# Kernel optimization log

Measured on AMD Instinct MI355X. Metric: run time of the kernel, lower is better.

Reference implementation:

```python
import jax, jax.numpy as jnp
import numpy as np

N = 100000   # nodes per type
E = 400000   # edges per relation
D = 128      # in_dim == out_dim
H = 4        # heads
DK = D // H  # 32
EPS = 1e-5


def setup_inputs() -> dict:
    key = jax.random.key(0)
    ks = jax.random.split(key, 16)
    s = 1.0 / np.sqrt(D)  # fan-in scaling for stable activations
    inp = {
        "x_drug": jax.random.normal(ks[0], (N, D), jnp.float32),
        "x_dis": jax.random.normal(ks[1], (N, D), jnp.float32),
        "Wp_drug": jax.random.normal(ks[2], (D, D), jnp.float32) * s,
        "bp_drug": jnp.zeros((D,), jnp.float32),
        "Wp_dis": jax.random.normal(ks[3], (D, D), jnp.float32) * s,
        "bp_dis": jnp.zeros((D,), jnp.float32),
        "Wk_r0": jax.random.normal(ks[4], (D, D), jnp.float32) * s,
        "Wv_r0": jax.random.normal(ks[5], (D, D), jnp.float32) * s,
        "Wk_r1": jax.random.normal(ks[6], (D, D), jnp.float32) * s,
        "Wv_r1": jax.random.normal(ks[7], (D, D), jnp.float32) * s,
        "Wu_drug": jax.random.normal(ks[8], (D, D), jnp.float32) * s,
        "bu_drug": jnp.zeros((D,), jnp.float32),
        "Wu_dis": jax.random.normal(ks[9], (D, D), jnp.float32) * s,
        "bu_dis": jnp.zeros((D,), jnp.float32),
        "g_drug": jnp.ones((D,), jnp.float32),
        "be_drug": jnp.zeros((D,), jnp.float32),
        "g_dis": jnp.ones((D,), jnp.float32),
        "be_dis": jnp.zeros((D,), jnp.float32),
        "ei_r0": jax.random.randint(ks[10], (2, E), 0, N, jnp.int32),  # drug -> dis
        "ei_r1": jax.random.randint(ks[11], (2, E), 0, N, jnp.int32),  # dis  -> drug
    }
    return inp


def _rel_attention(h_src_all, h_dst_all, ei, Wk, Wv, n_dst):
    # gather -> per-relation K/V proj -> edge softmax over dst -> scatter-add
    src, dst = ei[0], ei[1]
    h_src = h_src_all[src]                                  # [E, D]
    Q = h_dst_all[dst].reshape(-1, H, DK)                   # [E, H, DK]
    K = (h_src @ Wk).reshape(-1, H, DK)
    V = (h_src @ Wv).reshape(-1, H, DK)
    scores = jnp.sum(Q * K, axis=-1) / np.sqrt(DK)          # [E, H]
    # scatter_softmax over destination groups (numerically stable)
    m = jax.lax.stop_gradient(
        jax.ops.segment_max(scores, dst, num_segments=n_dst))  # [N, H]
    ex = jnp.exp(scores - m[dst])
    ssum = jax.ops.segment_sum(ex, dst, num_segments=n_dst)    # [N, H]
    attn = ex / ssum[dst]                                      # [E, H]
    wV = (V * attn[..., None]).reshape(-1, D)                  # [E, D]
    return jax.ops.segment_sum(wV, dst, num_segments=n_dst)    # [N, D]


def _update(h, agg, Wu, bu, g, be):
    x = h + (agg @ Wu + bu)  # skip + update (dropout=0)
    mu = jnp.mean(x, axis=-1, keepdims=True)
    var = jnp.var(x, axis=-1, keepdims=True)
    ln = (x - mu) * jax.lax.rsqrt(var + EPS) * g + be
    return jax.nn.relu(ln)


def reference(x_drug, x_dis, Wp_drug, bp_drug, Wp_dis, bp_dis,
              Wk_r0, Wv_r0, Wk_r1, Wv_r1,
              Wu_drug, bu_drug, Wu_dis, bu_dis,
              g_drug, be_drug, g_dis, be_dis, ei_r0, ei_r1):
    # type-specific projection
    h_drug = x_drug @ Wp_drug + bp_drug
    h_dis = x_dis @ Wp_dis + bp_dis
    # per-relation attention + intra/inter-type aggregation
    agg_dis = _rel_attention(h_drug, h_dis, ei_r0, Wk_r0, Wv_r0, N)
    agg_drug = _rel_attention(h_dis, h_drug, ei_r1, Wk_r1, Wv_r1, N)
    out_drug = _update(h_drug, agg_drug, Wu_drug, bu_drug, g_drug, be_drug)
    out_dis = _update(h_dis, agg_dis, Wu_dis, bu_dis, g_dis, be_dis)
    return jnp.stack([out_drug, out_dis])  # [2, N, D]
```

## Files before the change

### kernel.cpp

```cpp
#include <hip/hip_runtime.h>
#include <math.h>

#define NN 100000
#define EE 400000
#define DD 128

typedef __attribute__((ext_vector_type(8))) short bf16x8;
typedef __attribute__((ext_vector_type(4))) float f32x4;

#if defined(__has_builtin)
#if __has_builtin(__builtin_amdgcn_fdot2_f32_bf16)
#define HAVE_FDOT2 1
typedef __attribute__((ext_vector_type(2))) __bf16 bf16x2t;
#endif
#endif

__device__ __forceinline__ unsigned short f2bf(float f) {
  unsigned u = __float_as_uint(f);
  u += 0x7FFF + ((u >> 16) & 1);
  return (unsigned short)(u >> 16);
}
__device__ __forceinline__ float bf2f(unsigned short u) {
  return __uint_as_float(((unsigned)u) << 16);
}

__global__ __launch_bounds__(256) void prep_weights(
    const float* __restrict__ Wp_dr, const float* __restrict__ bp_dr,
    const float* __restrict__ Wp_di, const float* __restrict__ bp_di,
    const float* __restrict__ Wu_dr, const float* __restrict__ Wu_di,
    const float* __restrict__ Bk0, const float* __restrict__ Bv0,
    const float* __restrict__ Bk1, const float* __restrict__ Bv1,
    unsigned short* __restrict__ Wpt_dr, unsigned short* __restrict__ Wpt_di,
    unsigned short* __restrict__ Wut_dr, unsigned short* __restrict__ Wut_di,
    unsigned short* __restrict__ Wkt0, float* __restrict__ bk0,
    unsigned short* __restrict__ Wvt0, float* __restrict__ bv0,
    unsigned short* __restrict__ Wkt1, float* __restrict__ bk1,
    unsigned short* __restrict__ Wvt1, float* __restrict__ bv1) {
  const int b = blockIdx.x, t = threadIdx.x;
  if (b < 256) {
    const int id = b * 256 + t;
    const int m = id >> 14, rem = id & 16383, k = rem & 127, c = rem >> 7;
    const float* W = (m == 0) ? Wp_dr : (m == 1) ? Wp_di : (m == 2) ? Wu_dr : Wu_di;
    unsigned short* O = (m == 0) ? Wpt_dr : (m == 1) ? Wpt_di : (m == 2) ? Wut_dr : Wut_di;
    O[c * DD + k] = f2bf(W[(size_t)k * DD + c]);
  } else if (b < 512) {
    const int id = (b - 256) * 256 + t;
    const int m = id >> 14, rem = id & 16383, k = rem & 127, c = rem >> 7;
    const float* A = (m < 2) ? Wp_dr : Wp_di;
    const float* B = (m == 0) ? Bk0 : (m == 1) ? Bv0 : (m == 2) ? Bk1 : Bv1;
    unsigned short* O = (m == 0) ? Wkt0 : (m == 1) ? Wvt0 : (m == 2) ? Wkt1 : Wvt1;
    const float4* a4 = (const float4*)(A + (size_t)k * DD);
    float s = 0.0f;
#pragma unroll 8
    for (int j4 = 0; j4 < 32; ++j4) {
      const float4 av = a4[j4];
      s += av.x * B[(4 * j4 + 0) * DD + c] + av.y * B[(4 * j4 + 1) * DD + c]
         + av.z * B[(4 * j4 + 2) * DD + c] + av.w * B[(4 * j4 + 3) * DD + c];
    }
    O[c * DD + k] = f2bf(s);
  } else {
    const int id = (b - 512) * 256 + t;
    if (id < 512) {
      const int m = id >> 7, c = id & 127;
      const float* bp = (m < 2) ? bp_dr : bp_di;
      const float* B = (m == 0) ? Bk0 : (m == 1) ? Bv0 : (m == 2) ? Bk1 : Bv1;
      float* bo = (m == 0) ? bk0 : (m == 1) ? bv0 : (m == 2) ? bk1 : bv1;
      float s = 0.0f;
#pragma unroll 8
      for (int j = 0; j < DD; ++j) s += bp[j] * B[j * DD + c];
      bo[c] = s;
    }
  }
}

#define STAGE_W(SRC)                                                          \
  do {                                                                        \
    __syncthreads();                                                          \
    _Pragma("unroll") for (int i_ = threadIdx.x; i_ < 2048; i_ += 256) {      \
      const int L_ = i_ * 16;                                                 \
      *(float4*)((char*)WL + (L_ ^ (((L_ >> 8) & 7) << 4))) =                 \
          ((const float4*)(SRC))[i_];                                         \
    }                                                                         \
    __syncthreads();                                                          \
  } while (0)

__device__ __forceinline__ void mfma_tile_store(
    const unsigned short* WL, const bf16x8* a, int lane, int rowbase,
    bool wvalid, const float* __restrict__ bias,
    unsigned short* __restrict__ outb) {
  const int r0 = rowbase + (lane >> 4) * 4;
#pragma unroll
  for (int ni = 0; ni < 8; ++ni) {
    const int cl = ni * 16 + (lane & 15);
    f32x4 acc = {0.f, 0.f, 0.f, 0.f};
#pragma unroll
    for (int kk = 0; kk < 4; ++kk) {
      int boff = cl * 256 + kk * 64 + (lane >> 4) * 16;
      boff ^= (cl & 7) << 4;
      const bf16x8 bb = *(const bf16x8*)((const char*)WL + boff);
      acc = __builtin_amdgcn_mfma_f32_16x16x32_bf16(a[kk], bb, acc, 0, 0, 0);
    }
    if (wvalid) {
      const float bv = bias[cl];
#pragma unroll
      for (int r = 0; r < 4; ++r)
        outb[(size_t)(r0 + r) * DD + cl] = f2bf(acc[r] + bv);
    }
  }
}

__global__ __launch_bounds__(256) void fused_proj(
    const float* __restrict__ x0, const unsigned short* __restrict__ Wpt0,
    const float* __restrict__ bp0, const unsigned short* __restrict__ Wkta,
    const float* __restrict__ bka, const unsigned short* __restrict__ Wvta,
    const float* __restrict__ bva, unsigned short* __restrict__ h0,
    unsigned short* __restrict__ K0, unsigned short* __restrict__ V0,
    const float* __restrict__ x1, const unsigned short* __restrict__ Wpt1,
    const float* __restrict__ bp1, const unsigned short* __restrict__ Wktb,
    const float* __restrict__ bkb, const unsigned short* __restrict__ Wvtb,
    const float* __restrict__ bvb, unsigned short* __restrict__ h1,
    unsigned short* __restrict__ K1, unsigned short* __restrict__ V1, int half) {
  __shared__ unsigned short WL[DD * DD];
  int bid = blockIdx.x;
  const bool second = bid >= half;
  if (second) bid -= half;
  const float* x = second ? x1 : x0;
  const unsigned short* Wpt = second ? Wpt1 : Wpt0;
  const float* bpv = second ? bp1 : bp0;
  const unsigned short* Wkt = second ? Wktb : Wkta;
  const float* bkv = second ? bkb : bka;
  const unsigned short* Wvt = second ? Wvtb : Wvta;
  const float* bvv = second ? bvb : bva;
  unsigned short* h = second ? h1 : h0;
  unsigned short* K = second ? K1 : K0;
  unsigned short* V = second ? V1 : V0;

  const int tid = threadIdx.x, lane = tid & 63, wid = tid >> 6;
  const int rowbase = bid * 64 + wid * 16;
  const bool wvalid = rowbase < NN;
  bf16x8 a[4];
  if (wvalid) {
    const int arow = rowbase + (lane & 15);
    const float* xr = x + (size_t)arow * DD + (lane >> 4) * 8;
#pragma unroll
    for (int kk = 0; kk < 4; ++kk) {
      const float4 f0 = *(const float4*)(xr + kk * 32);
      const float4 f1 = *(const float4*)(xr + kk * 32 + 4);
      a[kk][0] = (short)f2bf(f0.x); a[kk][1] = (short)f2bf(f0.y);
      a[kk][2] = (short)f2bf(f0.z); a[kk][3] = (short)f2bf(f0.w);
      a[kk][4] = (short)f2bf(f1.x); a[kk][5] = (short)f2bf(f1.y);
      a[kk][6] = (short)f2bf(f1.z); a[kk][7] = (short)f2bf(f1.w);
    }
  } else {
#pragma unroll
    for (int kk = 0; kk < 4; ++kk)
#pragma unroll
      for (int j = 0; j < 8; ++j) a[kk][j] = 0;
  }
  STAGE_W(Wpt);
  mfma_tile_store(WL, a, lane, rowbase, wvalid, bpv, h);
  STAGE_W(Wkt);
  mfma_tile_store(WL, a, lane, rowbase, wvalid, bkv, K);
  STAGE_W(Wvt);
  mfma_tile_store(WL, a, lane, rowbase, wvalid, bvv, V);
}

__global__ __launch_bounds__(256) void update_ln2(
    const unsigned short* __restrict__ hA, const unsigned short* __restrict__ aggA,
    const unsigned short* __restrict__ WutA, const float* __restrict__ buA,
    const float* __restrict__ gA, const float* __restrict__ beA,
    float* __restrict__ outA,
    const unsigned short* __restrict__ hB, const unsigned short* __restrict__ aggB,
    const unsigned short* __restrict__ WutB, const float* __restrict__ buB,
    const float* __restrict__ gB, const float* __restrict__ beB,
    float* __restrict__ outB, int half) {
  __shared__ unsigned short WL[DD * DD];
  int bid = blockIdx.x;
  const bool second = bid >= half;
  if (second) bid -= half;
  const unsigned short* h = second ? hB : hA;
  const unsigned short* agg = second ? aggB : aggA;
  const unsigned short* Wut = second ? WutB : WutA;
  const float* bu = second ? buB : buA;
  const float* g = second ? gB : gA;
  const float* be = second ? beB : beA;
  float* out = second ? outB : outA;

  const int tid = threadIdx.x, lane = tid & 63, wid = tid >> 6;
  const int rowbase = bid * 64 + wid * 16;
  const bool wvalid = rowbase < NN;
  bf16x8 a[4];
  if (wvalid) {
    const int arow = rowbase + (lane & 15);
#pragma unroll
    for (int kk = 0; kk < 4; ++kk)
      a[kk] = *(const bf16x8*)(agg + (size_t)arow * DD + kk * 32 + (lane >> 4) * 8);
  } else {
#pragma unroll
    for (int kk = 0; kk < 4; ++kk)
#pragma unroll
      for (int j = 0; j < 8; ++j) a[kk][j] = 0;
  }
  STAGE_W(Wut);
  f32x4 acc[8];
  const int r0 = rowbase + (lane >> 4) * 4;
#pragma unroll
  for (int ni = 0; ni < 8; ++ni) {
    const int cl = ni * 16 + (lane & 15);
    acc[ni] = (f32x4){0.f, 0.f, 0.f, 0.f};
#pragma unroll
    for (int kk = 0; kk < 4; ++kk) {
      int boff = cl * 256 + kk * 64 + (lane >> 4) * 16;
      boff ^= (cl & 7) << 4;
      const bf16x8 bb = *(const bf16x8*)((const char*)WL + boff);
      acc[ni] = __builtin_amdgcn_mfma_f32_16x16x32_bf16(a[kk], bb, acc[ni], 0, 0, 0);
    }
  }
  if (!wvalid) return;
#pragma unroll
  for (int ni = 0; ni < 8; ++ni) {
    const int cl = ni * 16 + (lane & 15);
    const float bv = bu[cl];
#pragma unroll
    for (int r = 0; r < 4; ++r)
      acc[ni][r] += bf2f(h[(size_t)(r0 + r) * DD + cl]) + bv;
  }
  float mean[4], inv[4];
#pragma unroll
  for (int r = 0; r < 4; ++r) {
    float s = 0.f, q = 0.f;
#pragma unroll
    for (int ni = 0; ni < 8; ++ni) {
      const float v = acc[ni][r];
      s += v; q += v * v;
    }
    s += __shfl_xor(s, 1); q += __shfl_xor(q, 1);
    s += __shfl_xor(s, 2); q += __shfl_xor(q, 2);
    s += __shfl_xor(s, 4); q += __shfl_xor(q, 4);
    s += __shfl_xor(s, 8); q += __shfl_xor(q, 8);
    const float mu = s * (1.0f / 128.0f);
    mean[r] = mu;
    inv[r] = rsqrtf(q * (1.0f / 128.0f) - mu * mu + 1e-5f);
  }
#pragma unroll
  for (int ni = 0; ni < 8; ++ni) {
    const int cl = ni * 16 + (lane & 15);
    const float gv = g[cl], bev = be[cl];
#pragma unroll
    for (int r = 0; r < 4; ++r)
      out[(size_t)(r0 + r) * DD + cl] =
          fmaxf((acc[ni][r] - mean[r]) * inv[r] * gv + bev, 0.0f);
  }
}

__global__ __launch_bounds__(256) void count_deg2(const int* __restrict__ ei0,
                                                  const int* __restrict__ ei1,
                                                  int* __restrict__ deg) {
  const int e = blockIdx.x * 256 + threadIdx.x;
  if (e >= 2 * EE) return;
  const int d = (e < EE) ? ei0[EE + e] : (NN + ei1[e]);
  atomicAdd(&deg[d], 1);
}

__global__ __launch_bounds__(256) void scan1(const int* __restrict__ deg,
                                             int* __restrict__ excl,
                                             int* __restrict__ partials, int n) {
  __shared__ int ls[256];
  const int b0 = blockIdx.x * 1024;
  const int t = threadIdx.x;
  int v[4];
  int s = 0;
#pragma unroll
  for (int i = 0; i < 4; ++i) {
    const int idx = b0 + t * 4 + i;
    v[i] = (idx < n) ? deg[idx] : 0;
    s += v[i];
  }
  ls[t] = s;
  __syncthreads();
  for (int off = 1; off < 256; off <<= 1) {
    const int x = (t >= off) ? ls[t - off] : 0;
    __syncthreads();
    ls[t] += x;
    __syncthreads();
  }
  int ex = ls[t] - s;
#pragma unroll
  for (int i = 0; i < 4; ++i) {
    const int idx = b0 + t * 4 + i;
    if (idx < n) excl[idx] = ex;
    ex += v[i];
  }
  if (t == 255) partials[blockIdx.x] = ls[255];
}

__global__ __launch_bounds__(256) void scan2(int* __restrict__ partials, int nb) {
  __shared__ int ls[256];
  const int t = threadIdx.x;
  const int v = (t < nb) ? partials[t] : 0;
  ls[t] = v;
  __syncthreads();
  for (int off = 1; off < 256; off <<= 1) {
    const int x = (t >= off) ? ls[t - off] : 0;
    __syncthreads();
    ls[t] += x;
    __syncthreads();
  }
  if (t < nb) partials[t] = ls[t] - v;
}

__global__ __launch_bounds__(256) void scan3(const int* __restrict__ excl,
                                             const int* __restrict__ partials,
                                             int n, int* __restrict__ rowptr,
                                             int* __restrict__ cursor) {
  const int i = blockIdx.x * 256 + threadIdx.x;
  if (i < n) {
    const int v = excl[i] + partials[i >> 10];
    rowptr[i] = v;
    cursor[i] = v;
  }
  if (i == 0) rowptr[n] = 2 * EE;
}

__global__ __launch_bounds__(256) void fill_csr2(const int* __restrict__ ei0,
                                                 const int* __restrict__ ei1,
                                                 int* __restrict__ cursor,
                                                 int* __restrict__ csr_src) {
  const int e = blockIdx.x * 256 + threadIdx.x;
  if (e >= 2 * EE) return;
  int s, d;
  if (e < EE) { s = ei0[e]; d = ei0[EE + e]; }
  else        { s = ei1[e - EE]; d = NN + ei1[e]; }
  const int p = atomicAdd(&cursor[d], 1);
  csr_src[p] = s;
}

__global__ __launch_bounds__(256) void dst_attention(
    const unsigned short* __restrict__ Hq0, const unsigned short* __restrict__ K0,
    const unsigned short* __restrict__ V0, unsigned short* __restrict__ agg0,
    const unsigned short* __restrict__ Hq1, const unsigned short* __restrict__ K1,
    const unsigned short* __restrict__ V1, unsigned short* __restrict__ agg1,
    const int* __restrict__ rowptr, const int* __restrict__ csr_src) {
  const int gw = blockIdx.x * 4 + (threadIdx.x >> 6);
  if (gw >= 2 * NN) return;
  const bool rel1 = gw >= NN;
  const int node = rel1 ? gw - NN : gw;
  const unsigned short* Hq = rel1 ? Hq1 : Hq0;
  const unsigned short* K = rel1 ? K1 : K0;
  const unsigned short* V = rel1 ? V1 : V0;
  unsigned short* agg = rel1 ? agg1 : agg0;

  const int lane = threadIdx.x & 63;
  const int sub = lane & 15;
  const int grp = lane >> 4;
  const int beg = rowptr[gw], end = rowptr[gw + 1];
  const uint4 qu = *(const uint4*)(Hq + (size_t)node * DD + sub * 8);
#if defined(HAVE_FDOT2)
  const bf16x2t q0 = __builtin_bit_cast(bf16x2t, qu.x);
  const bf16x2t q1 = __builtin_bit_cast(bf16x2t, qu.y);
  const bf16x2t q2 = __builtin_bit_cast(bf16x2t, qu.z);
  const bf16x2t q3 = __builtin_bit_cast(bf16x2t, qu.w);
#else
  float qf[8];
  qf[0] = bf2f((unsigned short)qu.x); qf[1] = bf2f((unsigned short)(qu.x >> 16));
  qf[2] = bf2f((unsigned short)qu.y); qf[3] = bf2f((unsigned short)(qu.y >> 16));
  qf[4] = bf2f((unsigned short)qu.z); qf[5] = bf2f((unsigned short)(qu.z >> 16));
  qf[6] = bf2f((unsigned short)qu.w); qf[7] = bf2f((unsigned short)(qu.w >> 16));
#endif
  float av[8] = {0.f, 0.f, 0.f, 0.f, 0.f, 0.f, 0.f, 0.f};
  float lsum = 0.0f;
  for (int i = beg + grp; i < end; i += 4) {
    const int sidx = csr_src[i];
    const uint4 kp = *(const uint4*)(K + (size_t)sidx * DD + sub * 8);
#if defined(HAVE_FDOT2)
    float p = __builtin_amdgcn_fdot2_f32_bf16(__builtin_bit_cast(bf16x2t, kp.x), q0, 0.0f, false);
    p = __builtin_amdgcn_fdot2_f32_bf16(__builtin_bit_cast(bf16x2t, kp.y), q1, p, false);
    p = __builtin_amdgcn_fdot2_f32_bf16(__builtin_bit_cast(bf16x2t, kp.z), q2, p, false);
    p = __builtin_amdgcn_fdot2_f32_bf16(__builtin_bit_cast(bf16x2t, kp.w), q3, p, false);
#else
    float p;
    p  = qf[0] * bf2f((unsigned short)kp.x) + qf[1] * bf2f((unsigned short)(kp.x >> 16));
    p += qf[2] * bf2f((unsigned short)kp.y) + qf[3] * bf2f((unsigned short)(kp.y >> 16));
    p += qf[4] * bf2f((unsigned short)kp.z) + qf[5] * bf2f((unsigned short)(kp.z >> 16));
    p += qf[6] * bf2f((unsigned short)kp.w) + qf[7] * bf2f((unsigned short)(kp.w >> 16));
#endif
    p += __shfl_xor(p, 1);
    p += __shfl_xor(p, 2);
    const float wgt = __expf(p * 0.17677669529663689f);
    const uint4 vp = *(const uint4*)(V + (size_t)sidx * DD + sub * 8);
    lsum += wgt;
    av[0] += wgt * __uint_as_float(vp.x << 16);
    av[1] += wgt * __uint_as_float(vp.x & 0xFFFF0000u);
    av[2] += wgt * __uint_as_float(vp.y << 16);
    av[3] += wgt * __uint_as_float(vp.y & 0xFFFF0000u);
    av[4] += wgt * __uint_as_float(vp.z << 16);
    av[5] += wgt * __uint_as_float(vp.z & 0xFFFF0000u);
    av[6] += wgt * __uint_as_float(vp.w << 16);
    av[7] += wgt * __uint_as_float(vp.w & 0xFFFF0000u);
  }
#pragma unroll
  for (int d = 0; d < 8; ++d) {
    av[d] += __shfl_xor(av[d], 16);
    av[d] += __shfl_xor(av[d], 32);
  }
  lsum += __shfl_xor(lsum, 16);
  lsum += __shfl_xor(lsum, 32);
  if (grp == 0) {
    const float invl = (lsum > 0.0f) ? (1.0f / lsum) : 0.0f;
    uint4 o;
    o.x = (unsigned)f2bf(av[0] * invl) | ((unsigned)f2bf(av[1] * invl) << 16);
    o.y = (unsigned)f2bf(av[2] * invl) | ((unsigned)f2bf(av[3] * invl) << 16);
    o.z = (unsigned)f2bf(av[4] * invl) | ((unsigned)f2bf(av[5] * invl) << 16);
    o.w = (unsigned)f2bf(av[6] * invl) | ((unsigned)f2bf(av[7] * invl) << 16);
    *(uint4*)(agg + (size_t)node * DD + sub * 8) = o;
  }
}

extern "C" void kernel_launch(void* const* d_in, const int* in_sizes, int n_in,
                              void* d_out, int out_size, void* d_ws, size_t ws_size,
                              hipStream_t stream) {
  const float* x_drug  = (const float*)d_in[0];
  const float* x_dis   = (const float*)d_in[1];
  const float* Wp_drug = (const float*)d_in[2];
  const float* bp_drug = (const float*)d_in[3];
  const float* Wp_dis  = (const float*)d_in[4];
  const float* bp_dis  = (const float*)d_in[5];
  const float* Wk_r0   = (const float*)d_in[6];
  const float* Wv_r0   = (const float*)d_in[7];
  const float* Wk_r1   = (const float*)d_in[8];
  const float* Wv_r1   = (const float*)d_in[9];
  const float* Wu_drug = (const float*)d_in[10];
  const float* bu_drug = (const float*)d_in[11];
  const float* Wu_dis  = (const float*)d_in[12];
  const float* bu_dis  = (const float*)d_in[13];
  const float* g_drug  = (const float*)d_in[14];
  const float* be_drug = (const float*)d_in[15];
  const float* g_dis   = (const float*)d_in[16];
  const float* be_dis  = (const float*)d_in[17];
  const int* ei_r0     = (const int*)d_in[18];
  const int* ei_r1     = (const int*)d_in[19];

  float* out = (float*)d_out;
  float* out_drug = out;
  float* out_dis  = out + (size_t)NN * DD;

  const size_t ND = (size_t)NN * DD;
  char* w = (char*)d_ws;
  unsigned short* Kr0  = (unsigned short*)w; w += ND * 2;
  unsigned short* Vr0  = (unsigned short*)w; w += ND * 2;
  unsigned short* Kr1  = (unsigned short*)w; w += ND * 2;
  unsigned short* Vr1  = (unsigned short*)w; w += ND * 2;
  unsigned short* agdr = (unsigned short*)w; w += ND * 2;
  unsigned short* agdi = (unsigned short*)w; w += ND * 2;
  unsigned short* hb_dr = (unsigned short*)w; w += ND * 2;
  unsigned short* hb_di = (unsigned short*)w; w += ND * 2;
  unsigned short* Wpt_dr = (unsigned short*)w; w += DD * DD * 2;
  unsigned short* Wpt_di = (unsigned short*)w; w += DD * DD * 2;
  unsigned short* Wut_dr = (unsigned short*)w; w += DD * DD * 2;
  unsigned short* Wut_di = (unsigned short*)w; w += DD * DD * 2;
  unsigned short* Wkt0 = (unsigned short*)w; w += DD * DD * 2;
  unsigned short* Wvt0 = (unsigned short*)w; w += DD * DD * 2;
  unsigned short* Wkt1 = (unsigned short*)w; w += DD * DD * 2;
  unsigned short* Wvt1 = (unsigned short*)w; w += DD * DD * 2;
  float* bk0 = (float*)w; w += DD * 4;
  float* bv0 = (float*)w; w += DD * 4;
  float* bk1 = (float*)w; w += DD * 4;
  float* bv1 = (float*)w; w += DD * 4;
  int* deg      = (int*)w; w += 2 * NN * 4;
  int* excl     = (int*)w; w += 2 * NN * 4;
  int* rowptr   = (int*)w; w += (2 * NN + 1) * 4;
  int* cursor   = (int*)w; w += 2 * NN * 4;
  int* partials = (int*)w; w += 256 * 4;
  int* csr_src  = (int*)w; w += 2 * EE * 4;

  const int gemm_blocks = (NN + 63) / 64;
  const int edge_blocks2 = (2 * EE + 255) / 256;
  const int nchunks = (2 * NN + 1023) / 1024;
  const int n256 = (2 * NN + 255) / 256;
  const int attn_blocks = (2 * NN + 3) / 4;
  dim3 b256(256);

  prep_weights<<<514, b256, 0, stream>>>(
      Wp_drug, bp_drug, Wp_dis, bp_dis, Wu_drug, Wu_dis,
      Wk_r0, Wv_r0, Wk_r1, Wv_r1,
      Wpt_dr, Wpt_di, Wut_dr, Wut_di,
      Wkt0, bk0, Wvt0, bv0, Wkt1, bk1, Wvt1, bv1);

  fused_proj<<<2 * gemm_blocks, b256, 0, stream>>>(
      x_drug, Wpt_dr, bp_drug, Wkt0, bk0, Wvt0, bv0, hb_dr, Kr0, Vr0,
      x_dis,  Wpt_di, bp_dis,  Wkt1, bk1, Wvt1, bv1, hb_di, Kr1, Vr1,
      gemm_blocks);

  hipMemsetAsync(deg, 0, 2 * NN * sizeof(int), stream);
  count_deg2<<<edge_blocks2, b256, 0, stream>>>(ei_r0, ei_r1, deg);
  scan1<<<nchunks, b256, 0, stream>>>(deg, excl, partials, 2 * NN);
  scan2<<<1, b256, 0, stream>>>(partials, nchunks);
  scan3<<<n256, b256, 0, stream>>>(excl, partials, 2 * NN, rowptr, cursor);
  fill_csr2<<<edge_blocks2, b256, 0, stream>>>(ei_r0, ei_r1, cursor, csr_src);

  dst_attention<<<attn_blocks, b256, 0, stream>>>(
      hb_di, Kr0, Vr0, agdi,
      hb_dr, Kr1, Vr1, agdr,
      rowptr, csr_src);

  update_ln2<<<2 * gemm_blocks, b256, 0, stream>>>(
      hb_dr, agdr, Wut_dr, bu_drug, g_drug, be_drug, out_drug,
      hb_di, agdi, Wut_di, bu_dis,  g_dis,  be_dis,  out_dis,
      gemm_blocks);
}
```

Baseline: 300.0 us.

## Fuse degree counting into projection, zero deg in prep, double rows per wave, drop cursor

Folds the deg memset into prep_weights and the degree-count kernel into the fused_proj launch as extra blocks, which removes two launches. Each wave now computes two 16-row MFMA tiles, so every LDS weight fragment is reused twice, and the LDS swizzle widens from 8 to 16 rows. The separate cursor array is removed: fill_csr2 bumps rowptr in place, and attention recovers the row start as end minus deg. Register pressure is higher, and fewer blocks are launched for the GEMMs.

New measurement: 291.8 us. 1.03x faster.

```diff
diff --git a/kernel.cpp b/kernel.cpp
--- a/kernel.cpp
+++ b/kernel.cpp
@@ -35,7 +35,8 @@
     unsigned short* __restrict__ Wkt0, float* __restrict__ bk0,
     unsigned short* __restrict__ Wvt0, float* __restrict__ bv0,
     unsigned short* __restrict__ Wkt1, float* __restrict__ bk1,
-    unsigned short* __restrict__ Wvt1, float* __restrict__ bv1) {
+    unsigned short* __restrict__ Wvt1, float* __restrict__ bv1,
+    int* __restrict__ deg) {
   const int b = blockIdx.x, t = threadIdx.x;
   if (b < 256) {
     const int id = b * 256 + t;
@@ -58,7 +59,7 @@
          + av.z * B[(4 * j4 + 2) * DD + c] + av.w * B[(4 * j4 + 3) * DD + c];
     }
     O[c * DD + k] = f2bf(s);
-  } else {
+  } else if (b < 514) {
     const int id = (b - 512) * 256 + t;
     if (id < 512) {
       const int m = id >> 7, c = id & 127;
@@ -70,6 +71,9 @@
       for (int j = 0; j < DD; ++j) s += bp[j] * B[j * DD + c];
       bo[c] = s;
     }
+  } else {
+    const int id = (b - 514) * 256 + t;
+    if (id < 2 * NN) deg[id] = 0;
   }
 }
 
@@ -78,33 +82,60 @@
     __syncthreads();                                                          \
     _Pragma("unroll") for (int i_ = threadIdx.x; i_ < 2048; i_ += 256) {      \
       const int L_ = i_ * 16;                                                 \
-      *(float4*)((char*)WL + (L_ ^ (((L_ >> 8) & 7) << 4))) =                 \
+      *(float4*)((char*)WL + (L_ ^ (((L_ >> 8) & 15) << 4))) =                \
           ((const float4*)(SRC))[i_];                                         \
     }                                                                         \
     __syncthreads();                                                          \
   } while (0)
 
-__device__ __forceinline__ void mfma_tile_store(
-    const unsigned short* WL, const bf16x8* a, int lane, int rowbase,
-    bool wvalid, const float* __restrict__ bias,
+__device__ __forceinline__ void load_xfrag(const float* __restrict__ x,
+                                           int row, bool valid, int lane,
+                                           bf16x8* a) {
+  if (valid) {
+    const float* xr = x + (size_t)row * DD + (lane >> 4) * 8;
+#pragma unroll
+    for (int kk = 0; kk < 4; ++kk) {
+      const float4 f0 = *(const float4*)(xr + kk * 32);
+      const float4 f1 = *(const float4*)(xr + kk * 32 + 4);
+      a[kk][0] = (short)f2bf(f0.x); a[kk][1] = (short)f2bf(f0.y);
+      a[kk][2] = (short)f2bf(f0.z); a[kk][3] = (short)f2bf(f0.w);
+      a[kk][4] = (short)f2bf(f1.x); a[kk][5] = (short)f2bf(f1.y);
+      a[kk][6] = (short)f2bf(f1.z); a[kk][7] = (short)f2bf(f1.w);
+    }
+  } else {
+#pragma unroll
+    for (int kk = 0; kk < 4; ++kk)
+#pragma unroll
+      for (int j = 0; j < 8; ++j) a[kk][j] = 0;
+  }
+}
+
+__device__ __forceinline__ void mfma_tile_store2(
+    const unsigned short* WL, const bf16x8* a1, const bf16x8* a2, int lane,
+    int rowbase, bool v1, bool v2, const float* __restrict__ bias,
     unsigned short* __restrict__ outb) {
   const int r0 = rowbase + (lane >> 4) * 4;
 #pragma unroll
   for (int ni = 0; ni < 8; ++ni) {
     const int cl = ni * 16 + (lane & 15);
-    f32x4 acc = {0.f, 0.f, 0.f, 0.f};
+    f32x4 acc1 = {0.f, 0.f, 0.f, 0.f}, acc2 = {0.f, 0.f, 0.f, 0.f};
 #pragma unroll
     for (int kk = 0; kk < 4; ++kk) {
-      int boff = cl * 256 + kk * 64 + (lane >> 4) * 16;
-      boff ^= (cl & 7) << 4;
+      int boff = cl * 256 + ((kk * 64 + (lane >> 4) * 16) ^ ((cl & 15) << 4));
       const bf16x8 bb = *(const bf16x8*)((const char*)WL + boff);
-      acc = __builtin_amdgcn_mfma_f32_16x16x32_bf16(a[kk], bb, acc, 0, 0, 0);
-    }
-    if (wvalid) {
-      const float bv = bias[cl];
+      acc1 = __builtin_amdgcn_mfma_f32_16x16x32_bf16(a1[kk], bb, acc1, 0, 0, 0);
+      acc2 = __builtin_amdgcn_mfma_f32_16x16x32_bf16(a2[kk], bb, acc2, 0, 0, 0);
+    }
+    const float bv = bias[cl];
+    if (v1) {
 #pragma unroll
       for (int r = 0; r < 4; ++r)
-        outb[(size_t)(r0 + r) * DD + cl] = f2bf(acc[r] + bv);
+        outb[(size_t)(r0 + r) * DD + cl] = f2bf(acc1[r] + bv);
+    }
+    if (v2) {
+#pragma unroll
+      for (int r = 0; r < 4; ++r)
+        outb[(size_t)(r0 + 16 + r) * DD + cl] = f2bf(acc2[r] + bv);
     }
   }
 }
@@ -119,9 +150,21 @@
     const float* __restrict__ bp1, const unsigned short* __restrict__ Wktb,
     const float* __restrict__ bkb, const unsigned short* __restrict__ Wvtb,
     const float* __restrict__ bvb, unsigned short* __restrict__ h1,
-    unsigned short* __restrict__ K1, unsigned short* __restrict__ V1, int half) {
+    unsigned short* __restrict__ K1, unsigned short* __restrict__ V1,
+    int half, int cntblocks,
+    const int* __restrict__ ei0, const int* __restrict__ ei1,
+    int* __restrict__ deg) {
   __shared__ unsigned short WL[DD * DD];
   int bid = blockIdx.x;
+  if (bid < cntblocks) {
+    const int e = bid * 256 + threadIdx.x;
+    if (e < 2 * EE) {
+      const int d = (e < EE) ? ei0[EE + e] : (NN + ei1[e]);
+      atomicAdd(&deg[d], 1);
+    }
+    return;
+  }
+  bid -= cntblocks;
   const bool second = bid >= half;
   if (second) bid -= half;
   const float* x = second ? x1 : x0;
@@ -136,33 +179,17 @@
   unsigned short* V = second ? V1 : V0;
 
   const int tid = threadIdx.x, lane = tid & 63, wid = tid >> 6;
-  const int rowbase = bid * 64 + wid * 16;
-  const bool wvalid = rowbase < NN;
-  bf16x8 a[4];
-  if (wvalid) {
-    const int arow = rowbase + (lane & 15);
-    const float* xr = x + (size_t)arow * DD + (lane >> 4) * 8;
-#pragma unroll
-    for (int kk = 0; kk < 4; ++kk) {
-      const float4 f0 = *(const float4*)(xr + kk * 32);
-      const float4 f1 = *(const float4*)(xr + kk * 32 + 4);
-      a[kk][0] = (short)f2bf(f0.x); a[kk][1] = (short)f2bf(f0.y);
-      a[kk][2] = (short)f2bf(f0.z); a[kk][3] = (short)f2bf(f0.w);
-      a[kk][4] = (short)f2bf(f1.x); a[kk][5] = (short)f2bf(f1.y);
-      a[kk][6] = (short)f2bf(f1.z); a[kk][7] = (short)f2bf(f1.w);
-    }
-  } else {
-#pragma unroll
-    for (int kk = 0; kk < 4; ++kk)
-#pragma unroll
-      for (int j = 0; j < 8; ++j) a[kk][j] = 0;
-  }
+  const int rowbase = bid * 128 + wid * 32;
+  const bool v1 = rowbase < NN, v2 = rowbase + 16 < NN;
+  bf16x8 a1[4], a2[4];
+  load_xfrag(x, rowbase + (lane & 15), v1, lane, a1);
+  load_xfrag(x, rowbase + 16 + (lane & 15), v2, lane, a2);
   STAGE_W(Wpt);
-  mfma_tile_store(WL, a, lane, rowbase, wvalid, bpv, h);
+  mfma_tile_store2(WL, a1, a2, lane, rowbase, v1, v2, bpv, h);
   STAGE_W(Wkt);
-  mfma_tile_store(WL, a, lane, rowbase, wvalid, bkv, K);
+  mfma_tile_store2(WL, a1, a2, lane, rowbase, v1, v2, bkv, K);
   STAGE_W(Wvt);
-  mfma_tile_store(WL, a, lane, rowbase, wvalid, bvv, V);
+  mfma_tile_store2(WL, a1, a2, lane, rowbase, v1, v2, bvv, V);
 }
 
 __global__ __launch_bounds__(256) void update_ln2(
@@ -187,79 +214,78 @@
   float* out = second ? outB : outA;
 
   const int tid = threadIdx.x, lane = tid & 63, wid = tid >> 6;
-  const int rowbase = bid * 64 + wid * 16;
-  const bool wvalid = rowbase < NN;
-  bf16x8 a[4];
-  if (wvalid) {
-    const int arow = rowbase + (lane & 15);
-#pragma unroll
-    for (int kk = 0; kk < 4; ++kk)
-      a[kk] = *(const bf16x8*)(agg + (size_t)arow * DD + kk * 32 + (lane >> 4) * 8);
-  } else {
-#pragma unroll
-    for (int kk = 0; kk < 4; ++kk)
-#pragma unroll
-      for (int j = 0; j < 8; ++j) a[kk][j] = 0;
+  const int rowbase = bid * 128 + wid * 32;
+  const bool v1 = rowbase < NN, v2 = rowbase + 16 < NN;
+  const int ar1 = rowbase + (lane & 15), ar2 = ar1 + 16;
+  bf16x8 a1[4], a2[4];
+#pragma unroll
+  for (int kk = 0; kk < 4; ++kk) {
+    if (v1) a1[kk] = *(const bf16x8*)(agg + (size_t)ar1 * DD + kk * 32 + (lane >> 4) * 8);
+    else
+#pragma unroll
+      for (int j = 0; j < 8; ++j) a1[kk][j] = 0;
+    if (v2) a2[kk] = *(const bf16x8*)(agg + (size_t)ar2 * DD + kk * 32 + (lane >> 4) * 8);
+    else
+#pragma unroll
+      for (int j = 0; j < 8; ++j) a2[kk][j] = 0;
   }
   STAGE_W(Wut);
-  f32x4 acc[8];
+  f32x4 acc1[8], acc2[8];
   const int r0 = rowbase + (lane >> 4) * 4;
 #pragma unroll
   for (int ni = 0; ni < 8; ++ni) {
     const int cl = ni * 16 + (lane & 15);
-    acc[ni] = (f32x4){0.f, 0.f, 0.f, 0.f};
+    acc1[ni] = (f32x4){0.f, 0.f, 0.f, 0.f};
+    acc2[ni] = (f32x4){0.f, 0.f, 0.f, 0.f};
 #pragma unroll
     for (int kk = 0; kk < 4; ++kk) {
-      int boff = cl * 256 + kk * 64 + (lane >> 4) * 16;
-      boff ^= (cl & 7) << 4;
+      int boff = cl * 256 + ((kk * 64 + (lane >> 4) * 16) ^ ((cl & 15) << 4));
       const bf16x8 bb = *(const bf16x8*)((const char*)WL + boff);
-      acc[ni] = __builtin_amdgcn_mfma_f32_16x16x32_bf16(a[kk], bb, acc[ni], 0, 0, 0);
-    }
-  }
-  if (!wvalid) return;
-#pragma unroll
-  for (int ni = 0; ni < 8; ++ni) {
-    const int cl = ni * 16 + (lane & 15);
-    const float bv = bu[cl];
-#pragma unroll
-    for (int r = 0; r < 4; ++r)
-      acc[ni][r] += bf2f(h[(size_t)(r0 + r) * DD + cl]) + bv;
-  }
-  float mean[4], inv[4];
-#pragma unroll
-  for (int r = 0; r < 4; ++r) {
-    float s = 0.f, q = 0.f;
+      acc1[ni] = __builtin_amdgcn_mfma_f32_16x16x32_bf16(a1[kk], bb, acc1[ni], 0, 0, 0);
+      acc2[ni] = __builtin_amdgcn_mfma_f32_16x16x32_bf16(a2[kk], bb, acc2[ni], 0, 0, 0);
+    }
+  }
+  if (!v1) return;
+#pragma unroll
+  for (int set = 0; set < 2; ++set) {
+    if (set == 1 && !v2) break;
+    f32x4* acc = (set == 0) ? acc1 : acc2;
+    const int rb = r0 + set * 16;
 #pragma unroll
     for (int ni = 0; ni < 8; ++ni) {
-      const float v = acc[ni][r];
-      s += v; q += v * v;
-    }
-    s += __shfl_xor(s, 1); q += __shfl_xor(q, 1);
-    s += __shfl_xor(s, 2); q += __shfl_xor(q, 2);
-    s += __shfl_xor(s, 4); q += __shfl_xor(q, 4);
-    s += __shfl_xor(s, 8); q += __shfl_xor(q, 8);
-    const float mu = s * (1.0f / 128.0f);
-    mean[r] = mu;
-    inv[r] = rsqrtf(q * (1.0f / 128.0f) - mu * mu + 1e-5f);
-  }
-#pragma unroll
-  for (int ni = 0; ni < 8; ++ni) {
-    const int cl = ni * 16 + (lane & 15);
-    const float gv = g[cl], bev = be[cl];
-#pragma unroll
-    for (int r = 0; r < 4; ++r)
-      out[(size_t)(r0 + r) * DD + cl] =
-          fmaxf((acc[ni][r] - mean[r]) * inv[r] * gv + bev, 0.0f);
-  }
-}
-
-__global__ __launch_bounds__(256) void count_deg2(const int* __restrict__ ei0,
-                                                  const int* __restrict__ ei1,
-                                                  int* __restrict__ deg) {
-  const int e = blockIdx.x * 256 + threadIdx.x;
-  if (e >= 2 * EE) return;
-  const int d = (e < EE) ? ei0[EE + e] : (NN + ei1[e]);
-  atomicAdd(&deg[d], 1);
+      const int cl = ni * 16 + (lane & 15);
+      const float bv = bu[cl];
+#pragma unroll
+      for (int r = 0; r < 4; ++r)
+        acc[ni][r] += bf2f(h[(size_t)(rb + r) * DD + cl]) + bv;
+    }
+    float mean[4], inv[4];
+#pragma unroll
+    for (int r = 0; r < 4; ++r) {
+      float s = 0.f, q = 0.f;
+#pragma unroll
+      for (int ni = 0; ni < 8; ++ni) {
+        const float v = acc[ni][r];
+        s += v; q += v * v;
+      }
+      s += __shfl_xor(s, 1); q += __shfl_xor(q, 1);
+      s += __shfl_xor(s, 2); q += __shfl_xor(q, 2);
+      s += __shfl_xor(s, 4); q += __shfl_xor(q, 4);
+      s += __shfl_xor(s, 8); q += __shfl_xor(q, 8);
+      const float mu = s * (1.0f / 128.0f);
+      mean[r] = mu;
+      inv[r] = rsqrtf(q * (1.0f / 128.0f) - mu * mu + 1e-5f);
+    }
+#pragma unroll
+    for (int ni = 0; ni < 8; ++ni) {
+      const int cl = ni * 16 + (lane & 15);
+      const float gv = g[cl], bev = be[cl];
+#pragma unroll
+      for (int r = 0; r < 4; ++r)
+        out[(size_t)(rb + r) * DD + cl] =
+            fmaxf((acc[ni][r] - mean[r]) * inv[r] * gv + bev, 0.0f);
+    }
+  }
 }
 
 __global__ __launch_bounds__(256) void scan1(const int* __restrict__ deg,
@@ -311,27 +337,21 @@
 
 __global__ __launch_bounds__(256) void scan3(const int* __restrict__ excl,
                                              const int* __restrict__ partials,
-                                             int n, int* __restrict__ rowptr,
-                                             int* __restrict__ cursor) {
+                                             int n, int* __restrict__ rowptr) {
   const int i = blockIdx.x * 256 + threadIdx.x;
-  if (i < n) {
-    const int v = excl[i] + partials[i >> 10];
-    rowptr[i] = v;
-    cursor[i] = v;
-  }
-  if (i == 0) rowptr[n] = 2 * EE;
+  if (i < n) rowptr[i] = excl[i] + partials[i >> 10];
 }
 
 __global__ __launch_bounds__(256) void fill_csr2(const int* __restrict__ ei0,
                                                  const int* __restrict__ ei1,
-                                                 int* __restrict__ cursor,
+                                                 int* __restrict__ rowptr,
                                                  int* __restrict__ csr_src) {
   const int e = blockIdx.x * 256 + threadIdx.x;
   if (e >= 2 * EE) return;
   int s, d;
   if (e < EE) { s = ei0[e]; d = ei0[EE + e]; }
   else        { s = ei1[e - EE]; d = NN + ei1[e]; }
-  const int p = atomicAdd(&cursor[d], 1);
+  const int p = atomicAdd(&rowptr[d], 1);
   csr_src[p] = s;
 }
 
@@ -340,7 +360,8 @@
     const unsigned short* __restrict__ V0, unsigned short* __restrict__ agg0,
     const unsigned short* __restrict__ Hq1, const unsigned short* __restrict__ K1,
     const unsigned short* __restrict__ V1, unsigned short* __restrict__ agg1,
-    const int* __restrict__ rowptr, const int* __restrict__ csr_src) {
+    const int* __restrict__ rowptr, const int* __restrict__ deg,
+    const int* __restrict__ csr_src) {
   const int gw = blockIdx.x * 4 + (threadIdx.x >> 6);
   if (gw >= 2 * NN) return;
   const bool rel1 = gw >= NN;
@@ -353,7 +374,8 @@
   const int lane = threadIdx.x & 63;
   const int sub = lane & 15;
   const int grp = lane >> 4;
-  const int beg = rowptr[gw], end = rowptr[gw + 1];
+  const int end = rowptr[gw];
+  const int beg = end - deg[gw];
   const uint4 qu = *(const uint4*)(Hq + (size_t)node * DD + sub * 8);
 #if defined(HAVE_FDOT2)
   const bf16x2t q0 = __builtin_bit_cast(bf16x2t, qu.x);
@@ -469,42 +491,40 @@
   int* deg      = (int*)w; w += 2 * NN * 4;
   int* excl     = (int*)w; w += 2 * NN * 4;
   int* rowptr   = (int*)w; w += (2 * NN + 1) * 4;
-  int* cursor   = (int*)w; w += 2 * NN * 4;
   int* partials = (int*)w; w += 256 * 4;
   int* csr_src  = (int*)w; w += 2 * EE * 4;
 
-  const int gemm_blocks = (NN + 63) / 64;
-  const int edge_blocks2 = (2 * EE + 255) / 256;
+  const int proj_half = (NN + 127) / 128;
+  const int cnt_blocks = (2 * EE + 255) / 256;
   const int nchunks = (2 * NN + 1023) / 1024;
   const int n256 = (2 * NN + 255) / 256;
   const int attn_blocks = (2 * NN + 3) / 4;
+  const int zero_blocks = (2 * NN + 255) / 256;
   dim3 b256(256);
 
-  prep_weights<<<514, b256, 0, stream>>>(
+  prep_weights<<<514 + zero_blocks, b256, 0, stream>>>(
       Wp_drug, bp_drug, Wp_dis, bp_dis, Wu_drug, Wu_dis,
       Wk_r0, Wv_r0, Wk_r1, Wv_r1,
       Wpt_dr, Wpt_di, Wut_dr, Wut_di,
-      Wkt0, bk0, Wvt0, bv0, Wkt1, bk1, Wvt1, bv1);
-
-  fused_proj<<<2 * gemm_blocks, b256, 0, stream>>>(
+      Wkt0, bk0, Wvt0, bv0, Wkt1, bk1, Wvt1, bv1, deg);
+
+  fused_proj<<<cnt_blocks + 2 * proj_half, b256, 0, stream>>>(
       x_drug, Wpt_dr, bp_drug, Wkt0, bk0, Wvt0, bv0, hb_dr, Kr0, Vr0,
       x_dis,  Wpt_di, bp_dis,  Wkt1, bk1, Wvt1, bv1, hb_di, Kr1, Vr1,
-      gemm_blocks);
-
-  hipMemsetAsync(deg, 0, 2 * NN * sizeof(int), stream);
-  count_deg2<<<edge_blocks2, b256, 0, stream>>>(ei_r0, ei_r1, deg);
+      proj_half, cnt_blocks, ei_r0, ei_r1, deg);
+
   scan1<<<nchunks, b256, 0, stream>>>(deg, excl, partials, 2 * NN);
   scan2<<<1, b256, 0, stream>>>(partials, nchunks);
-  scan3<<<n256, b256, 0, stream>>>(excl, partials, 2 * NN, rowptr, cursor);
-  fill_csr2<<<edge_blocks2, b256, 0, stream>>>(ei_r0, ei_r1, cursor, csr_src);
+  scan3<<<n256, b256, 0, stream>>>(excl, partials, 2 * NN, rowptr);
+  fill_csr2<<<cnt_blocks, b256, 0, stream>>>(ei_r0, ei_r1, rowptr, csr_src);
 
   dst_attention<<<attn_blocks, b256, 0, stream>>>(
       hb_di, Kr0, Vr0, agdi,
       hb_dr, Kr1, Vr1, agdr,
-      rowptr, csr_src);
-
-  update_ln2<<<2 * gemm_blocks, b256, 0, stream>>>(
+      rowptr, deg, csr_src);
+
+  update_ln2<<<2 * proj_half, b256, 0, stream>>>(
       hb_dr, agdr, Wut_dr, bu_drug, g_drug, be_drug, out_drug,
       hb_di, agdi, Wut_di, bu_dis,  g_dis,  be_dis,  out_dis,
-      gemm_blocks);
-}
+      proj_half);
+}
```
